# Optimization experiments

Measured on AMD Instinct MI355X. Metric: run time of the kernel, lower is better.

The kernel has to match this reference:

```python
import jax, jax.numpy as jnp
import numpy as np

B, H, L, D = 4, 8, 2048, 64
FACTOR = 5


def setup_inputs() -> dict:
    key = jax.random.key(0)
    kq, kk, kv, ki = jax.random.split(key, 4)
    sample_k = min(FACTOR * int(np.ceil(np.log(L))), L)  # = 40
    queries = jax.random.normal(kq, (B, H, L, D), jnp.float32)
    keys = jax.random.normal(kk, (B, H, L, D), jnp.float32)
    values = jax.random.normal(kv, (B, H, L, D), jnp.float32)
    index_sample = jax.random.randint(ki, (L, sample_k), 0, L)
    return {"queries": queries, "keys": keys, "values": values,
            "index_sample": index_sample}


def prob_attention(queries, keys, values, index_sample):
    Bq, Hq, L_Q, Dk = queries.shape
    L_K = keys.shape[2]
    n_top = min(FACTOR * int(np.ceil(np.log(L_Q))), L_Q)  # u
    scale = float(1.0 / np.sqrt(Dk))

    # --- _prob_QK: sample scores for each query over random key subset ---
    # K_sample: (B,H,L_Q,S,D); index_sample shared across batch/heads
    K_sample = keys[:, :, index_sample, :]
    Q_K_sample = jnp.einsum('bhld,bhlsd->bhls', queries, K_sample)
    # sparsity measure M = max - mean (mean over full L_K as in source)
    M = Q_K_sample.max(-1) - Q_K_sample.sum(-1) / L_K      # (B,H,L_Q)
    M_top = jax.lax.top_k(M, n_top)[1]                     # (B,H,u) query indices

    # full scores only for the selected "active" queries
    Q_reduce = jnp.take_along_axis(queries, M_top[..., None], axis=2)  # (B,H,u,D)
    scores = jnp.einsum('bhud,bhkd->bhuk', Q_reduce, keys) * scale     # (B,H,u,L_K)

    # --- causal ProbMask: key j masked when j > selected query position ---
    causal = jnp.arange(L_K)[None, None, None, :] > M_top[..., None]
    scores = jnp.where(causal, -jnp.inf, scores)
    attn = jax.nn.softmax(scores, axis=-1)
    ctx_update = jnp.einsum('bhuk,bhkd->bhud', attn, values)           # (B,H,u,D)

    # --- initial context (causal branch): running cumulative sum of V ---
    context = jnp.cumsum(values, axis=2)                               # (B,H,L_Q,D)

    # scatter active-query results back into the context
    b_idx = jnp.arange(Bq)[:, None, None]
    h_idx = jnp.arange(Hq)[None, :, None]
    context = context.at[b_idx, h_idx, M_top].set(ctx_update)
    return context


def reference(queries, keys, values, index_sample):
    return prob_attention(queries, keys, values, index_sample)
```

## Files before the change

### kernel.cpp

```cpp
#include <hip/hip_runtime.h>
#include <hip/hip_bf16.h>
#include <cstdint>

#define BB 4
#define HH 8
#define LL 2048
#define DD 64
#define SK 40
#define NT 40
#define BHN (BB*HH)
#define SCALE 0.125f
#define CHUNK 128
#define NCH (LL/CHUNK)
#define USPL 2
#define UPB (NT/USPL)

#define WS_M    0
#define WS_SUB  (WS_M + BHN*LL)
#define WS_CTX  (WS_SUB + BHN*64*DD)
#define WS_PM   (WS_CTX + BHN*NT*DD)
#define WS_PSUM (WS_PM + BHN*NT*NCH)
#define WS_PACC (WS_PSUM + BHN*NT*NCH)
#define WS_TOP  (WS_PACC + BHN*NT*NCH*DD)

__global__ __launch_bounds__(256) void k1_M(const float* __restrict__ Q,
                                            const float* __restrict__ K,
                                            const int* __restrict__ isamp,
                                            float* __restrict__ M) {
    int bid  = blockIdx.x;
    int swz  = (bid & 7) * (BHN * LL / 4 / 8) + (bid >> 3);
    int wid  = swz * 4 + (threadIdx.x >> 6);
    int lane = threadIdx.x & 63;
    int bh   = wid >> 11;
    int l    = wid & (LL - 1);
    int g    = lane >> 4;
    int e    = lane & 15;

    float4 q = reinterpret_cast<const float4*>(Q + (size_t)wid * DD)[e];
    const float* Kbh = K + (size_t)bh * LL * DD;
    const int* irow = isamp + l * SK;

    int idxs[SK / 4];
#pragma unroll
    for (int p = 0; p < SK / 4; p++) idxs[p] = irow[p * 4 + g];

    float mx = -INFINITY, sm = 0.f;
#pragma unroll
    for (int b = 0; b < 2; b++) {
        float4 kv[5];
#pragma unroll
        for (int i = 0; i < 5; i++)
            kv[i] = reinterpret_cast<const float4*>(Kbh + (size_t)idxs[b * 5 + i] * DD)[e];
        float dd[5];
#pragma unroll
        for (int i = 0; i < 5; i++)
            dd[i] = q.x * kv[i].x + q.y * kv[i].y + q.z * kv[i].z + q.w * kv[i].w;
#pragma unroll
        for (int i = 0; i < 5; i++) {
            float d = dd[i];
            d += __shfl_xor(d, 1);
            d += __shfl_xor(d, 2);
            d += __shfl_xor(d, 4);
            d += __shfl_xor(d, 8);
            mx = fmaxf(mx, d);
            sm += d;
        }
    }
    mx = fmaxf(mx, __shfl_xor(mx, 16));
    mx = fmaxf(mx, __shfl_xor(mx, 32));
    sm += __shfl_xor(sm, 16);
    sm += __shfl_xor(sm, 32);
    if (lane == 0) M[wid] = mx - sm * (1.0f / (float)LL);
}

__global__ __launch_bounds__(64) void k2_topk(const float* __restrict__ M,
                                              int* __restrict__ Mtop) {
    int bh = blockIdx.x, lane = threadIdx.x;
    const float* Mb = M + (size_t)bh * LL;
    unsigned long long key[32];
#pragma unroll
    for (int j = 0; j < 32; j++) {
        int i = lane + j * 64;
        unsigned u = __float_as_uint(Mb[i]);
        u = (u & 0x80000000u) ? ~u : (u | 0x80000000u);
        key[j] = ((unsigned long long)u << 32) | (unsigned)(~i);
    }
    unsigned long long winner = 0ull;
    for (int t = 0; t < NT; t++) {
        unsigned long long best = 0ull;
#pragma unroll
        for (int j = 0; j < 32; j++) {
            unsigned long long k = key[j];
            k = (k == winner) ? 0ull : k;
            key[j] = k;
            best = (k > best) ? k : best;
        }
#pragma unroll
        for (int off = 32; off; off >>= 1) {
            unsigned long long o = __shfl_xor(best, off);
            best = (o > best) ? o : best;
        }
        winner = best;
        if (lane == 0) Mtop[bh * NT + t] = (int)(~(unsigned)(best & 0xFFFFFFFFull));
    }
}

__global__ __launch_bounds__(256) void k3a_partial(const float* __restrict__ Q,
                                                   const float* __restrict__ K,
                                                   const float* __restrict__ V,
                                                   const int* __restrict__ Mtop,
                                                   float* __restrict__ pm,
                                                   float* __restrict__ psum,
                                                   float* __restrict__ pacc) {
    __shared__ float q_lds[UPB * DD];
    __shared__ float s_lds[UPB][CHUNK];
    __shared__ int   qi_lds[UPB];
    int bid = blockIdx.x;
    int swz = (bid & 7) * (BHN * NCH * USPL / 8) + (bid >> 3);
    int bh  = swz >> 5;
    int rem = swz & 31;
    int ch  = rem >> 1;
    int u0  = (rem & 1) * UPB;
    int ck  = ch * CHUNK;
    int tid = threadIdx.x;

    if (tid < UPB) qi_lds[tid] = Mtop[bh * NT + u0 + tid];
    __syncthreads();
    for (int c = tid; c < UPB * 16; c += 256) {
        int u = c >> 4, j = c & 15;
        reinterpret_cast<float4*>(q_lds)[c] =
            reinterpret_cast<const float4*>(Q + ((size_t)bh * LL + qi_lds[u]) * DD)[j];
    }
    __syncthreads();

    int k    = ck + (tid >> 1);
    int half = tid & 1;
    const float4* krow = reinterpret_cast<const float4*>(K + ((size_t)bh * LL + k) * DD) + half * 8;
    float4 kreg[8];
#pragma unroll
    for (int j = 0; j < 8; j++) kreg[j] = krow[j];
    for (int u = 0; u < UPB; u++) {
        const float4* q4 = reinterpret_cast<const float4*>(q_lds + u * DD) + half * 8;
        float d = 0.f;
#pragma unroll
        for (int j = 0; j < 8; j++) {
            float4 a = q4[j], b = kreg[j];
            d += a.x * b.x + a.y * b.y + a.z * b.z + a.w * b.w;
        }
        d += __shfl_xor(d, 1);
        float s = (k <= qi_lds[u]) ? d * SCALE : -INFINITY;
        if (half == 0) s_lds[u][k - ck] = s;
    }
    __syncthreads();

    int w = tid >> 6, lane = tid & 63;
#pragma unroll
    for (int uu = 0; uu < UPB / 4; uu++) {
        int u = w + uu * 4;
        float s0 = s_lds[u][lane], s1 = s_lds[u][lane + 64];
        float m = fmaxf(s0, s1);
#pragma unroll
        for (int off = 32; off; off >>= 1) m = fmaxf(m, __shfl_xor(m, off));
        float e0 = (s0 == -INFINITY) ? 0.f : __expf(s0 - m);
        float e1 = (s1 == -INFINITY) ? 0.f : __expf(s1 - m);
        s_lds[u][lane] = e0;
        s_lds[u][lane + 64] = e1;
        float smv = e0 + e1;
#pragma unroll
        for (int off = 32; off; off >>= 1) smv += __shfl_xor(smv, off);
        if (lane == 0) {
            size_t rg = (size_t)bh * NT + u0 + u;
            pm  [rg * NCH + ch] = m;
            psum[rg * NCH + ch] = smv;
        }
    }
    __syncthreads();

    float acc[UPB / 4] = {};
    const float* vbase = V + ((size_t)bh * LL + ck) * DD + lane;
#pragma unroll 4
    for (int kk = 0; kk < CHUNK; kk++) {
        float v = vbase[(size_t)kk * DD];
#pragma unroll
        for (int uu = 0; uu < UPB / 4; uu++)
            acc[uu] += s_lds[w + uu * 4][kk] * v;
    }
#pragma unroll
    for (int uu = 0; uu < UPB / 4; uu++) {
        size_t rg = (size_t)bh * NT + u0 + w + uu * 4;
        pacc[(rg * NCH + ch) * DD + lane] = acc[uu];
    }
}

__global__ __launch_bounds__(64) void k4a_sub(const float* __restrict__ V,
                                              float* __restrict__ sub) {
    int blk = blockIdx.x;
    int lane = threadIdx.x;
    size_t base = (size_t)blk * 32 * DD + lane;
    float acc = 0.f;
#pragma unroll 8
    for (int r = 0; r < 32; r++) acc += V[base + (size_t)r * DD];
    sub[(size_t)blk * DD + lane] = acc;
}

__global__ __launch_bounds__(64) void k4b_scan(const float* __restrict__ V,
                                               const float* __restrict__ sub,
                                               float* __restrict__ out) {
    int blk = blockIdx.x;
    int bh = blk >> 6, j = blk & 63;
    int lane = threadIdx.x;
    float off = 0.f;
    for (int p = 0; p < j; p++) off += sub[((size_t)(bh * 64 + p)) * DD + lane];
    size_t base = (size_t)blk * 32 * DD + lane;
    float acc = off;
    for (int r = 0; r < 32; r++) {
        acc += V[base + (size_t)r * DD];
        out[base + (size_t)r * DD] = acc;
    }
}

__global__ __launch_bounds__(64) void k3b_scatter(const float* __restrict__ pm,
                                                  const float* __restrict__ psum,
                                                  const float* __restrict__ pacc,
                                                  const int* __restrict__ Mtop,
                                                  float* __restrict__ out) {
    int row = blockIdx.x;
    int lane = threadIdx.x;
    int bh = row / NT;
    float pmv[NCH];
    float m = -INFINITY;
#pragma unroll
    for (int i = 0; i < NCH; i++) {
        pmv[i] = pm[(size_t)row * NCH + i];
        m = fmaxf(m, pmv[i]);
    }
    float Z = 0.f, acc = 0.f;
#pragma unroll
    for (int i = 0; i < NCH; i++) {
        float sc = (pmv[i] == -INFINITY) ? 0.f : __expf(pmv[i] - m);
        Z   += psum[(size_t)row * NCH + i] * sc;
        acc += pacc[((size_t)row * NCH + i) * DD + lane] * sc;
    }
    int qi = Mtop[row];
    out[((size_t)bh * LL + qi) * DD + lane] = acc / Z;
}

extern "C" void kernel_launch(void* const* d_in, const int* in_sizes, int n_in,
                              void* d_out, int out_size, void* d_ws, size_t ws_size,
                              hipStream_t stream) {
    const float* Q = (const float*)d_in[0];
    const float* K = (const float*)d_in[1];
    const float* V = (const float*)d_in[2];
    const int* isamp = (const int*)d_in[3];
    float* ws   = (float*)d_ws;
    float* M    = ws + WS_M;
    float* sub  = ws + WS_SUB;
    float* pm   = ws + WS_PM;
    float* psum = ws + WS_PSUM;
    float* pacc = ws + WS_PACC;
    int*   Mtop = (int*)(ws + WS_TOP);
    float* out  = (float*)d_out;

    k1_M       <<<BHN * LL / 4,       256, 0, stream>>>(Q, K, isamp, M);
    k2_topk    <<<BHN,                 64, 0, stream>>>(M, Mtop);
    k3a_partial<<<BHN * NCH * USPL,   256, 0, stream>>>(Q, K, V, Mtop, pm, psum, pacc);
    k4a_sub    <<<BHN * 64,            64, 0, stream>>>(V, sub);
    k4b_scan   <<<BHN * 64,            64, 0, stream>>>(V, sub, out);
    k3b_scatter<<<BHN * NT,            64, 0, stream>>>(pm, psum, pacc, Mtop, out);
}
```

Baseline: 202.7 us.

## Fuse scatter into cumsum scan, vectorize scan kernels, split queries finer in partial

```diff
diff --git a/kernel.cpp b/kernel.cpp
--- a/kernel.cpp
+++ b/kernel.cpp
@@ -12,7 +12,7 @@
 #define SCALE 0.125f
 #define CHUNK 128
 #define NCH (LL/CHUNK)
-#define USPL 2
+#define USPL 5
 #define UPB (NT/USPL)
 
 #define WS_M    0
@@ -22,6 +22,10 @@
 #define WS_PSUM (WS_PM + BHN*NT*NCH)
 #define WS_PACC (WS_PSUM + BHN*NT*NCH)
 #define WS_TOP  (WS_PACC + BHN*NT*NCH*DD)
+
+static __device__ __forceinline__ float4 f4add(float4 a, float4 b) {
+    float4 r; r.x = a.x + b.x; r.y = a.y + b.y; r.z = a.z + b.z; r.w = a.w + b.w; return r;
+}
 
 __global__ __launch_bounds__(256) void k1_M(const float* __restrict__ Q,
                                             const float* __restrict__ K,
@@ -117,10 +121,10 @@
     __shared__ int   qi_lds[UPB];
     int bid = blockIdx.x;
     int swz = (bid & 7) * (BHN * NCH * USPL / 8) + (bid >> 3);
-    int bh  = swz >> 5;
-    int rem = swz & 31;
-    int ch  = rem >> 1;
-    int u0  = (rem & 1) * UPB;
+    int bh  = swz / (NCH * USPL);
+    int rem = swz % (NCH * USPL);
+    int ch  = rem / USPL;
+    int u0  = (rem % USPL) * UPB;
     int ck  = ch * CHUNK;
     int tid = threadIdx.x;
 
@@ -139,6 +143,7 @@
     float4 kreg[8];
 #pragma unroll
     for (int j = 0; j < 8; j++) kreg[j] = krow[j];
+#pragma unroll
     for (int u = 0; u < UPB; u++) {
         const float4* q4 = reinterpret_cast<const float4*>(q_lds + u * DD) + half * 8;
         float d = 0.f;
@@ -192,57 +197,78 @@
     }
 }
 
-__global__ __launch_bounds__(64) void k4a_sub(const float* __restrict__ V,
-                                              float* __restrict__ sub) {
+__global__ __launch_bounds__(256) void k4a_sub(const float* __restrict__ V,
+                                               float* __restrict__ sub) {
+    __shared__ float4 part[16][16];
     int blk = blockIdx.x;
-    int lane = threadIdx.x;
-    size_t base = (size_t)blk * 32 * DD + lane;
-    float acc = 0.f;
-#pragma unroll 8
-    for (int r = 0; r < 32; r++) acc += V[base + (size_t)r * DD];
-    sub[(size_t)blk * DD + lane] = acc;
-}
-
-__global__ __launch_bounds__(64) void k4b_scan(const float* __restrict__ V,
-                                               const float* __restrict__ sub,
-                                               float* __restrict__ out) {
+    int t = threadIdx.x;
+    int d4 = t & 15, rg = t >> 4;
+    const float4* v4 = reinterpret_cast<const float4*>(V) + (size_t)blk * 32 * 16 + (size_t)rg * 2 * 16 + d4;
+    float4 a = v4[0], b = v4[16];
+    part[rg][d4] = f4add(a, b);
+    __syncthreads();
+#pragma unroll
+    for (int step = 8; step; step >>= 1) {
+        if (rg < step) part[rg][d4] = f4add(part[rg][d4], part[rg + step][d4]);
+        __syncthreads();
+    }
+    if (rg == 0)
+        reinterpret_cast<float4*>(sub)[(size_t)blk * 16 + d4] = part[0][d4];
+}
+
+__global__ __launch_bounds__(256) void k4b_scan(const float* __restrict__ V,
+                                                const float* __restrict__ sub,
+                                                const float* __restrict__ pm,
+                                                const float* __restrict__ psum,
+                                                const float* __restrict__ pacc,
+                                                const int* __restrict__ Mtop,
+                                                float* __restrict__ out) {
+    __shared__ float4 plds[16][16];
     int blk = blockIdx.x;
     int bh = blk >> 6, j = blk & 63;
-    int lane = threadIdx.x;
-    float off = 0.f;
-    for (int p = 0; p < j; p++) off += sub[((size_t)(bh * 64 + p)) * DD + lane];
-    size_t base = (size_t)blk * 32 * DD + lane;
-    float acc = off;
-    for (int r = 0; r < 32; r++) {
-        acc += V[base + (size_t)r * DD];
-        out[base + (size_t)r * DD] = acc;
-    }
-}
-
-__global__ __launch_bounds__(64) void k3b_scatter(const float* __restrict__ pm,
-                                                  const float* __restrict__ psum,
-                                                  const float* __restrict__ pacc,
-                                                  const int* __restrict__ Mtop,
-                                                  float* __restrict__ out) {
-    int row = blockIdx.x;
-    int lane = threadIdx.x;
-    int bh = row / NT;
-    float pmv[NCH];
-    float m = -INFINITY;
-#pragma unroll
-    for (int i = 0; i < NCH; i++) {
-        pmv[i] = pm[(size_t)row * NCH + i];
-        m = fmaxf(m, pmv[i]);
-    }
-    float Z = 0.f, acc = 0.f;
-#pragma unroll
-    for (int i = 0; i < NCH; i++) {
-        float sc = (pmv[i] == -INFINITY) ? 0.f : __expf(pmv[i] - m);
-        Z   += psum[(size_t)row * NCH + i] * sc;
-        acc += pacc[((size_t)row * NCH + i) * DD + lane] * sc;
-    }
-    int qi = Mtop[row];
-    out[((size_t)bh * LL + qi) * DD + lane] = acc / Z;
+    int t = threadIdx.x;
+    int d4 = t & 15, rg = t >> 4;
+
+    const float4* sub4 = reinterpret_cast<const float4*>(sub) + (size_t)(bh * 64) * 16 + d4;
+    float4 off = {0.f, 0.f, 0.f, 0.f};
+    for (int p = 0; p < j; p++) off = f4add(off, sub4[(size_t)p * 16]);
+
+    const float4* v4 = reinterpret_cast<const float4*>(V) + (size_t)blk * 32 * 16 + (size_t)rg * 2 * 16 + d4;
+    float4 a = v4[0], b = v4[16];
+    plds[rg][d4] = f4add(a, b);
+    __syncthreads();
+    float4 ex = {0.f, 0.f, 0.f, 0.f};
+    for (int p = 0; p < rg; p++) ex = f4add(ex, plds[p][d4]);
+
+    float4 r0 = f4add(f4add(off, ex), a);
+    float4 r1 = f4add(r0, b);
+    float4* o4 = reinterpret_cast<float4*>(out) + (size_t)blk * 32 * 16 + (size_t)rg * 2 * 16 + d4;
+    o4[0] = r0;
+    o4[16] = r1;
+    __syncthreads();
+
+    if (t < DD) {
+        for (int u = 0; u < NT; u++) {
+            int qi = Mtop[bh * NT + u];
+            if ((qi >> 5) != j) continue;
+            size_t row = (size_t)bh * NT + u;
+            float pmv[NCH];
+            float m = -INFINITY;
+#pragma unroll
+            for (int i = 0; i < NCH; i++) {
+                pmv[i] = pm[row * NCH + i];
+                m = fmaxf(m, pmv[i]);
+            }
+            float Z = 0.f, acc = 0.f;
+#pragma unroll
+            for (int i = 0; i < NCH; i++) {
+                float sc = (pmv[i] == -INFINITY) ? 0.f : __expf(pmv[i] - m);
+                Z   += psum[row * NCH + i] * sc;
+                acc += pacc[(row * NCH + i) * DD + t] * sc;
+            }
+            out[((size_t)bh * LL + qi) * DD + t] = acc / Z;
+        }
+    }
 }
 
 extern "C" void kernel_launch(void* const* d_in, const int* in_sizes, int n_in,
@@ -261,10 +287,9 @@
     int*   Mtop = (int*)(ws + WS_TOP);
     float* out  = (float*)d_out;
 
-    k1_M       <<<BHN * LL / 4,       256, 0, stream>>>(Q, K, isamp, M);
-    k2_topk    <<<BHN,                 64, 0, stream>>>(M, Mtop);
-    k3a_partial<<<BHN * NCH * USPL,   256, 0, stream>>>(Q, K, V, Mtop, pm, psum, pacc);
-    k4a_sub    <<<BHN * 64,            64, 0, stream>>>(V, sub);
-    k4b_scan   <<<BHN * 64,            64, 0, stream>>>(V, sub, out);
-    k3b_scatter<<<BHN * NT,            64, 0, stream>>>(pm, psum, pacc, Mtop, out);
-}
+    k1_M       <<<BHN * LL / 4,      256, 0, stream>>>(Q, K, isamp, M);
+    k2_topk    <<<BHN,                64, 0, stream>>>(M, Mtop);
+    k3a_partial<<<BHN * NCH * USPL,  256, 0, stream>>>(Q, K, V, Mtop, pm, psum, pacc);
+    k4a_sub    <<<BHN * 64,          256, 0, stream>>>(V, sub);
+    k4b_scan   <<<BHN * 64,          256, 0, stream>>>(V, sub, pm, psum, pacc, Mtop, out);
+}
```

New measurement: 213.0 us. +5.0%, slower.
